# Performance work log

Hardware: AMD Instinct MI355X
Metric: run time of the kernel (lower is better)

Reference implementation:

```python
import math
import jax, jax.numpy as jnp
import numpy as np

B, T, E, H = 4, 2048, 256, 8
OBS_DIM, ACT_DIM = 17, 6
JOINED = OBS_DIM + ACT_DIM + 2  # 25: transition width in TAP trajectory transformer


def setup_inputs() -> dict:
    key = jax.random.key(0)
    ks = jax.random.split(key, 5)
    s = 0.02
    return {
        "x": jax.random.normal(ks[0], (B, T, E), dtype=jnp.float32),
        "Wq": jax.random.normal(ks[1], (E, E), dtype=jnp.float32) * s,
        "bq": jnp.zeros((E,), jnp.float32),
        "Wk": jax.random.normal(ks[2], (E, E), dtype=jnp.float32) * s,
        "bk": jnp.zeros((E,), jnp.float32),
        "Wv": jax.random.normal(ks[3], (E, E), dtype=jnp.float32) * s,
        "bv": jnp.zeros((E,), jnp.float32),
        "Wo": jax.random.normal(ks[4], (E, E), dtype=jnp.float32) * s,
        "bo": jnp.zeros((E,), jnp.float32),
    }


def _mask(t):
    # causal tril with every JOINED-th column (the "done"/boundary token) zeroed
    m = jnp.tril(jnp.ones((t, t), dtype=bool))
    keep_col = (jnp.arange(t) % JOINED) != (JOINED - 1)
    return m & keep_col[None, :]  # (t, t)


def reference(x, Wq, bq, Wk, bk, Wv, bv, Wo, bo):
    b, t, e = x.shape
    d = e // H
    # torch nn.Linear: y = x @ W.T + b
    q = (x @ Wq.T + bq).reshape(b, t, H, d).transpose(0, 2, 1, 3)  # b h t d
    k = (x @ Wk.T + bk).reshape(b, t, H, d).transpose(0, 2, 1, 3)
    v = (x @ Wv.T + bv).reshape(b, t, H, d).transpose(0, 2, 1, 3)

    scores = jnp.einsum("bhtd,bhsd->bhts", q, k) * (1.0 / math.sqrt(d))
    scores = jnp.where(_mask(t)[None, None], scores, -jnp.inf)
    attn = jax.nn.softmax(scores, axis=-1)  # (b, h, t, t) — dropout rate 0 => identity
    out = jnp.einsum("bhts,bhsd->bhtd", attn, v)  # b h t d
    out = out.transpose(0, 2, 1, 3).reshape(b, t, e)  # b t (h d)
    return out @ Wo.T + bo
```

## Files before the change

### kernel.cpp

```cpp
#include <hip/hip_runtime.h>

#define BB 4
#define TT 2048
#define EE 256
#define HH 8
#define DD 32
#define JOINED 25
#define CSCALE 0.2550539239731586f

typedef __attribute__((ext_vector_type(8))) __bf16 bf16x8;
typedef __attribute__((ext_vector_type(4))) float f32x4;

static __device__ __forceinline__ unsigned short f2bf(float f) {
    unsigned u = __float_as_uint(f);
    u += 0x7fffu + ((u >> 16) & 1u);
    return (unsigned short)(u >> 16);
}
static __device__ __forceinline__ unsigned pk2bf(float a, float b) {
    return (unsigned)f2bf(a) | ((unsigned)f2bf(b) << 16);
}

union BF8U { uint4 u; bf16x8 b; };
static __device__ __forceinline__ bf16x8 ld_frag(const unsigned short* p) {
    BF8U t; t.u = *(const uint4*)p; return t.b;
}

#define MFMA(a, b, c) __builtin_amdgcn_mfma_f32_16x16x32_bf16((a), (b), (c), 0, 0, 0)

__global__ __launch_bounds__(256) void prep_kernel(
    const float* __restrict__ x,
    const float* __restrict__ Wq, const float* __restrict__ Wk,
    const float* __restrict__ Wv, const float* __restrict__ Wo,
    unsigned short* __restrict__ xb, unsigned short* __restrict__ wqb,
    unsigned short* __restrict__ wkb, unsigned short* __restrict__ wvb,
    unsigned short* __restrict__ wob, unsigned short* __restrict__ onesG)
{
    const size_t NX = (size_t)BB * TT * EE;
    const size_t NMAIN = NX + 4 * (size_t)EE * EE;
    size_t idx = ((size_t)blockIdx.x * 256 + threadIdx.x) * 8;
    if (idx >= NMAIN) {
        size_t base = idx - NMAIN;
        #pragma unroll
        for (int i = 0; i < 8; ++i) {
            size_t e = base + i;
            if (e < (size_t)JOINED * 64) {
                int phase = (int)(e >> 6), o = (int)(e & 63);
                onesG[e] = (((phase + o) % JOINED) != (JOINED - 1)) ? (unsigned short)0x3F80
                                                                    : (unsigned short)0;
            }
        }
        return;
    }
    const float* src; unsigned short* dst; size_t off;
    if (idx < NX) { src = x; dst = xb; off = idx; }
    else {
        size_t i2 = idx - NX;
        int wsel = (int)(i2 >> 16);
        off = i2 & 65535u;
        src = wsel == 0 ? Wq : wsel == 1 ? Wk : wsel == 2 ? Wv : Wo;
        dst = wsel == 0 ? wqb : wsel == 1 ? wkb : wsel == 2 ? wvb : wob;
    }
    float4 a = *(const float4*)(src + off);
    float4 b = *(const float4*)(src + off + 4);
    uint4 o;
    o.x = pk2bf(a.x, a.y); o.y = pk2bf(a.z, a.w);
    o.z = pk2bf(b.x, b.y); o.w = pk2bf(b.z, b.w);
    *(uint4*)(dst + off) = o;
}

__global__ __launch_bounds__(256) void qkv_kernel(
    const unsigned short* __restrict__ xb,
    const unsigned short* __restrict__ wall,
    const float* __restrict__ bq, const float* __restrict__ bk,
    const float* __restrict__ bv,
    unsigned short* __restrict__ qo, unsigned short* __restrict__ ko,
    unsigned short* __restrict__ vto)
{
    __shared__ unsigned short As[128*136];
    __shared__ unsigned short Bs[128*136];

    const int m0 = blockIdx.x * 128;
    const int n0 = blockIdx.y * 128;
    const int which = blockIdx.y >> 1;
    const float* __restrict__ bias = which == 0 ? bq : which == 1 ? bk : bv;

    const int tid = threadIdx.x;
    const int w = tid >> 6, lane = tid & 63, quad = lane >> 4, lq = lane & 15;
    const int wm = (w & 1) * 64, wn = (w >> 1) * 64;
    const int srow = tid >> 4, scol = (tid & 15) * 8;

    f32x4 acc[4][4] = {};

    for (int k0 = 0; k0 < EE; k0 += 128) {
        __syncthreads();
        #pragma unroll
        for (int i = 0; i < 8; ++i) {
            int r = i * 16 + srow;
            *(uint4*)&As[r*136 + scol] = *(const uint4*)&xb  [(size_t)(m0 + r)*EE + k0 + scol];
            *(uint4*)&Bs[r*136 + scol] = *(const uint4*)&wall[(size_t)(n0 + r)*EE + k0 + scol];
        }
        __syncthreads();
        #pragma unroll
        for (int ks = 0; ks < 4; ++ks) {
            bf16x8 af[4], bfr[4];
            #pragma unroll
            for (int t = 0; t < 4; ++t) {
                af[t]  = ld_frag(&As[(wm + t*16 + lq)*136 + ks*32 + quad*8]);
                bfr[t] = ld_frag(&Bs[(wn + t*16 + lq)*136 + ks*32 + quad*8]);
            }
            #pragma unroll
            for (int mi = 0; mi < 4; ++mi)
                #pragma unroll
                for (int f = 0; f < 4; ++f)
                    acc[mi][f] = MFMA(af[mi], bfr[f], acc[mi][f]);
        }
    }

    #pragma unroll
    for (int f = 0; f < 4; ++f) {
        int nf = (n0 + wn + f*16 + lq) & 255;
        int h = nf >> 5, d = nf & 31;
        float bb = bias[nf];
        #pragma unroll
        for (int mi = 0; mi < 4; ++mi) {
            int t0 = m0 + wm + mi*16 + quad*4;
            int b = t0 >> 11, tl = t0 & (TT - 1);
            if (which == 0) {
                #pragma unroll
                for (int reg = 0; reg < 4; ++reg)
                    qo[(((size_t)b*HH + h)*TT + tl + reg)*DD + d] =
                        f2bf((acc[mi][f][reg] + bb) * CSCALE);
            } else if (which == 1) {
                #pragma unroll
                for (int reg = 0; reg < 4; ++reg)
                    ko[(((size_t)b*HH + h)*TT + tl + reg)*DD + d] =
                        f2bf(acc[mi][f][reg] + bb);
            } else {
                int r25 = tl % JOINED;
                int mreg = (JOINED - 1) - r25;
                float vv[4];
                #pragma unroll
                for (int reg = 0; reg < 4; ++reg)
                    vv[reg] = (reg == mreg) ? 0.f : (acc[mi][f][reg] + bb);
                uint2 pk;
                pk.x = pk2bf(vv[0], vv[1]);
                pk.y = pk2bf(vv[2], vv[3]);
                *(uint2*)&vto[(((size_t)b*HH + h)*DD + d)*TT + tl] = pk;
            }
        }
    }
}

__global__ __launch_bounds__(256, 4) void attn_kernel(
    const unsigned short* __restrict__ q, const unsigned short* __restrict__ k,
    const unsigned short* __restrict__ vt, const unsigned short* __restrict__ onesG,
    unsigned short* __restrict__ ao)
{
    __shared__ unsigned short Ks[2][64*40];
    __shared__ unsigned short Vt[2][32*72];
    __shared__ unsigned short Ps[4][16*72];

    const int L = blockIdx.x;
    const int xcd   = L & 7;
    const int inner = L >> 3;
    const int bh = xcd * 4 + (inner & 3);
    const int iq = 31 - (inner >> 2);
    const int b = bh >> 3, hh = bh & 7;

    const int tid = threadIdx.x;
    const int w = tid >> 6, lane = tid & 63, quad = lane >> 4, lq = lane & 15;
    const int r0 = iq * 64;
    const int q0 = r0 + w*16;
    const int ntiles = iq + 1;

    const int rk = tid >> 2, ck = (tid & 3) * 8;
    const int rv = tid >> 3, cv = (tid & 7) * 8;

    const unsigned short* qb_ = q  + (size_t)bh * TT * DD;
    const unsigned short* kb_ = k  + (size_t)bh * TT * DD;
    const unsigned short* vb_ = vt + (size_t)bh * DD * TT;

    const bf16x8 qf = ld_frag(qb_ + (size_t)(q0 + lq)*DD + quad*8);

    {
        uint4 kreg = *(const uint4*)(kb_ + (size_t)rk*DD + ck);
        uint4 vreg = *(const uint4*)(vb_ + (size_t)rv*TT + cv);
        *(uint4*)&Ks[0][rk*40 + ck] = kreg;
        *(uint4*)&Vt[0][rv*72 + cv] = vreg;
    }
    __syncthreads();

    f32x4 O0 = {0,0,0,0}, O1 = {0,0,0,0}, Ld = {0,0,0,0};
    int phase = 0;

    for (int jt = 0; jt < ntiles; ++jt) {
        const int j0 = jt * 64;
        const int jn = (jt + 1 < ntiles) ? j0 + 64 : j0;
        uint4 kreg = *(const uint4*)(kb_ + (size_t)(jn + rk)*DD + ck);
        uint4 vreg = *(const uint4*)(vb_ + (size_t)rv*TT + jn + cv);

        bf16x8 ones0 = ld_frag(&onesG[phase*64 +      quad*8]);
        bf16x8 ones1 = ld_frag(&onesG[phase*64 + 32 + quad*8]);

        const unsigned short* Kb = &Ks[jt & 1][0];
        const unsigned short* Vb = &Vt[jt & 1][0];

        f32x4 St[4];
        #pragma unroll
        for (int f = 0; f < 4; ++f) {
            bf16x8 kf = ld_frag(&Kb[(f*16 + lq)*40 + quad*8]);
            f32x4 z = {0,0,0,0};
            St[f] = MFMA(kf, qf, z);
        }
        if (jt == ntiles - 1) {
            int row = q0 + lq;
            #pragma unroll
            for (int f = 0; f < 4; ++f) {
                int kvb = j0 + f*16 + quad*4;
                #pragma unroll
                for (int reg = 0; reg < 4; ++reg)
                    St[f][reg] = (kvb + reg <= row) ? St[f][reg] : -1e30f;
            }
        }
        unsigned short* ps = &Ps[w][0];
        #pragma unroll
        for (int f = 0; f < 4; ++f) {
            float p0 = __builtin_amdgcn_exp2f(St[f][0]);
            float p1 = __builtin_amdgcn_exp2f(St[f][1]);
            float p2 = __builtin_amdgcn_exp2f(St[f][2]);
            float p3 = __builtin_amdgcn_exp2f(St[f][3]);
            uint2 pk;
            pk.x = pk2bf(p0, p1);
            pk.y = pk2bf(p2, p3);
            *(uint2*)&ps[lq*72 + f*16 + quad*4] = pk;
        }
        #pragma unroll
        for (int c = 0; c < 2; ++c) {
            bf16x8 pa  = ld_frag(&ps[lq*72 + c*32 + quad*8]);
            bf16x8 v0f = ld_frag(&Vb[(lq)*72      + c*32 + quad*8]);
            bf16x8 v1f = ld_frag(&Vb[(16 + lq)*72 + c*32 + quad*8]);
            O0 = MFMA(pa, v0f, O0);
            O1 = MFMA(pa, v1f, O1);
            Ld = MFMA(pa, (c ? ones1 : ones0), Ld);
        }

        *(uint4*)&Ks[(jt + 1) & 1][rk*40 + ck] = kreg;
        *(uint4*)&Vt[(jt + 1) & 1][rv*72 + cv] = vreg;
        __syncthreads();

        phase += 14; if (phase >= JOINED) phase -= JOINED;
    }

    #pragma unroll
    for (int reg = 0; reg < 4; ++reg) {
        float inv = 1.0f / Ld[reg];
        int t = q0 + quad*4 + reg;
        size_t ob = ((size_t)b*TT + t)*EE + hh*DD;
        ao[ob + lq]      = f2bf(O0[reg] * inv);
        ao[ob + 16 + lq] = f2bf(O1[reg] * inv);
    }
}

__global__ __launch_bounds__(256) void proj_kernel(
    const unsigned short* __restrict__ a, const unsigned short* __restrict__ W,
    const float* __restrict__ bias, float* __restrict__ out)
{
    __shared__ unsigned short As[128*136];
    __shared__ unsigned short Bs[128*136];

    const int m0 = blockIdx.x * 128;
    const int n0 = blockIdx.y * 128;
    const int tid = threadIdx.x;
    const int w = tid >> 6, lane = tid & 63, quad = lane >> 4, lq = lane & 15;
    const int wm = (w & 1) * 64, wn = (w >> 1) * 64;
    const int srow = tid >> 4, scol = (tid & 15) * 8;

    f32x4 acc[4][4] = {};

    for (int k0 = 0; k0 < EE; k0 += 128) {
        __syncthreads();
        #pragma unroll
        for (int i = 0; i < 8; ++i) {
            int r = i * 16 + srow;
            *(uint4*)&As[r*136 + scol] = *(const uint4*)&a[(size_t)(m0 + r)*EE + k0 + scol];
            *(uint4*)&Bs[r*136 + scol] = *(const uint4*)&W[(size_t)(n0 + r)*EE + k0 + scol];
        }
        __syncthreads();
        #pragma unroll
        for (int ks = 0; ks < 4; ++ks) {
            bf16x8 af[4], bfr[4];
            #pragma unroll
            for (int t = 0; t < 4; ++t) {
                af[t]  = ld_frag(&As[(wm + t*16 + lq)*136 + ks*32 + quad*8]);
                bfr[t] = ld_frag(&Bs[(wn + t*16 + lq)*136 + ks*32 + quad*8]);
            }
            #pragma unroll
            for (int mi = 0; mi < 4; ++mi)
                #pragma unroll
                for (int f = 0; f < 4; ++f)
                    acc[mi][f] = MFMA(af[mi], bfr[f], acc[mi][f]);
        }
    }

    #pragma unroll
    for (int f = 0; f < 4; ++f) {
        int n = n0 + wn + f*16 + lq;
        float bb = bias[n];
        #pragma unroll
        for (int mi = 0; mi < 4; ++mi) {
            int m = m0 + wm + mi*16 + quad*4;
            #pragma unroll
            for (int reg = 0; reg < 4; ++reg)
                out[(size_t)(m + reg)*EE + n] = acc[mi][f][reg] + bb;
        }
    }
}

extern "C" void kernel_launch(void* const* d_in, const int* in_sizes, int n_in,
                              void* d_out, int out_size, void* d_ws, size_t ws_size,
                              hipStream_t stream) {
    const float* x  = (const float*)d_in[0];
    const float* Wq = (const float*)d_in[1];
    const float* bq = (const float*)d_in[2];
    const float* Wk = (const float*)d_in[3];
    const float* bk = (const float*)d_in[4];
    const float* Wv = (const float*)d_in[5];
    const float* bv = (const float*)d_in[6];
    const float* Wo = (const float*)d_in[7];
    const float* bo = (const float*)d_in[8];
    float* out = (float*)d_out;

    const size_t n_elem = (size_t)BB * TT * EE;
    const size_t w_elem = (size_t)EE * EE;
    unsigned short* xb    = (unsigned short*)d_ws;
    unsigned short* wqb   = xb  + n_elem;
    unsigned short* wkb   = wqb + w_elem;
    unsigned short* wvb   = wkb + w_elem;
    unsigned short* wob   = wvb + w_elem;
    unsigned short* qq    = wob + w_elem;
    unsigned short* kk    = qq  + n_elem;
    unsigned short* vtt   = kk  + n_elem;
    unsigned short* ao    = vtt + n_elem;
    unsigned short* onesG = ao  + n_elem;

    const int prep_blocks = (int)((n_elem + 4*w_elem) / 2048) + 1;
    prep_kernel<<<dim3(prep_blocks), 256, 0, stream>>>(
        x, Wq, Wk, Wv, Wo, xb, wqb, wkb, wvb, wob, onesG);
    qkv_kernel <<<dim3(BB*TT/128, 6), 256, 0, stream>>>(
        xb, wqb, bq, bk, bv, qq, kk, vtt);
    attn_kernel<<<dim3(1024), 256, 0, stream>>>(qq, kk, vtt, onesG, ao);
    proj_kernel<<<dim3(BB*TT/128, EE/128), 256, 0, stream>>>(ao, wob, bo, out);
}
```

Measured before the change: 120.5 us.

## Split causal attention KV range into chunks with a separate merge kernel

The attention kernel now splits each query tile's key range into chunks of up to 8 KV tiles, giving 2560 blocks of roughly equal work instead of 1024 blocks with very uneven causal lengths. Each block writes unnormalized fp32 partial outputs and row sums to a workspace buffer. A new merge kernel adds the partials and normalizes before the output projection. Because softmax is computed without a running max, the partials can simply be summed. The costs are extra global traffic for the partials, one more kernel launch, and dropping the previous XCD-aware block ordering.

```diff
diff --git a/kernel.cpp b/kernel.cpp
--- a/kernel.cpp
+++ b/kernel.cpp
@@ -7,6 +7,9 @@
 #define DD 32
 #define JOINED 25
 #define CSCALE 0.2550539239731586f
+#define PROW 33
+#define PCHUNK (64*PROW)
+#define PART_OFF (64u << 20)
 
 typedef __attribute__((ext_vector_type(8))) __bf16 bf16x8;
 typedef __attribute__((ext_vector_type(4))) float f32x4;
@@ -154,24 +157,27 @@
 __global__ __launch_bounds__(256, 4) void attn_kernel(
     const unsigned short* __restrict__ q, const unsigned short* __restrict__ k,
     const unsigned short* __restrict__ vt, const unsigned short* __restrict__ onesG,
-    unsigned short* __restrict__ ao)
+    float* __restrict__ part)
 {
     __shared__ unsigned short Ks[2][64*40];
     __shared__ unsigned short Vt[2][32*72];
     __shared__ unsigned short Ps[4][16*72];
 
     const int L = blockIdx.x;
-    const int xcd   = L & 7;
-    const int inner = L >> 3;
-    const int bh = xcd * 4 + (inner & 3);
-    const int iq = 31 - (inner >> 2);
-    const int b = bh >> 3, hh = bh & 7;
+    const int bh = L & 31;
+    const int widx = L >> 5;
+    int iq, c;
+    if (widx < 8)       { iq = widx;               c = 0; }
+    else if (widx < 24) { int t = widx - 8;  iq = 8  + (t >> 1); c = t & 1; }
+    else if (widx < 48) { int t = widx - 24; iq = 16 + t / 3;    c = t % 3; }
+    else                { int t = widx - 48; iq = 24 + (t >> 2); c = t & 3; }
+    const int tstart = c * 8;
+    const int tend = min(tstart + 8, iq + 1);
 
     const int tid = threadIdx.x;
     const int w = tid >> 6, lane = tid & 63, quad = lane >> 4, lq = lane & 15;
     const int r0 = iq * 64;
     const int q0 = r0 + w*16;
-    const int ntiles = iq + 1;
 
     const int rk = tid >> 2, ck = (tid & 3) * 8;
     const int rv = tid >> 3, cv = (tid & 7) * 8;
@@ -183,19 +189,19 @@
     const bf16x8 qf = ld_frag(qb_ + (size_t)(q0 + lq)*DD + quad*8);
 
     {
-        uint4 kreg = *(const uint4*)(kb_ + (size_t)rk*DD + ck);
-        uint4 vreg = *(const uint4*)(vb_ + (size_t)rv*TT + cv);
+        uint4 kreg = *(const uint4*)(kb_ + (size_t)(tstart*64 + rk)*DD + ck);
+        uint4 vreg = *(const uint4*)(vb_ + (size_t)rv*TT + tstart*64 + cv);
         *(uint4*)&Ks[0][rk*40 + ck] = kreg;
         *(uint4*)&Vt[0][rv*72 + cv] = vreg;
     }
     __syncthreads();
 
     f32x4 O0 = {0,0,0,0}, O1 = {0,0,0,0}, Ld = {0,0,0,0};
-    int phase = 0;
-
-    for (int jt = 0; jt < ntiles; ++jt) {
+    int phase = (tstart * 64) % JOINED;
+
+    for (int jt = tstart; jt < tend; ++jt) {
         const int j0 = jt * 64;
-        const int jn = (jt + 1 < ntiles) ? j0 + 64 : j0;
+        const int jn = (jt + 1 < tend) ? j0 + 64 : j0;
         uint4 kreg = *(const uint4*)(kb_ + (size_t)(jn + rk)*DD + ck);
         uint4 vreg = *(const uint4*)(vb_ + (size_t)rv*TT + jn + cv);
 
@@ -212,7 +218,7 @@
             f32x4 z = {0,0,0,0};
             St[f] = MFMA(kf, qf, z);
         }
-        if (jt == ntiles - 1) {
+        if (jt == iq) {
             int row = q0 + lq;
             #pragma unroll
             for (int f = 0; f < 4; ++f) {
@@ -235,13 +241,13 @@
             *(uint2*)&ps[lq*72 + f*16 + quad*4] = pk;
         }
         #pragma unroll
-        for (int c = 0; c < 2; ++c) {
-            bf16x8 pa  = ld_frag(&ps[lq*72 + c*32 + quad*8]);
-            bf16x8 v0f = ld_frag(&Vb[(lq)*72      + c*32 + quad*8]);
-            bf16x8 v1f = ld_frag(&Vb[(16 + lq)*72 + c*32 + quad*8]);
+        for (int cc = 0; cc < 2; ++cc) {
+            bf16x8 pa  = ld_frag(&ps[lq*72 + cc*32 + quad*8]);
+            bf16x8 v0f = ld_frag(&Vb[(lq)*72      + cc*32 + quad*8]);
+            bf16x8 v1f = ld_frag(&Vb[(16 + lq)*72 + cc*32 + quad*8]);
             O0 = MFMA(pa, v0f, O0);
             O1 = MFMA(pa, v1f, O1);
-            Ld = MFMA(pa, (c ? ones1 : ones0), Ld);
+            Ld = MFMA(pa, (cc ? ones1 : ones0), Ld);
         }
 
         *(uint4*)&Ks[(jt + 1) & 1][rk*40 + ck] = kreg;
@@ -251,14 +257,37 @@
         phase += 14; if (phase >= JOINED) phase -= JOINED;
     }
 
+    float* pb = part + ((size_t)(bh*32 + iq)*4 + c) * PCHUNK;
     #pragma unroll
     for (int reg = 0; reg < 4; ++reg) {
-        float inv = 1.0f / Ld[reg];
-        int t = q0 + quad*4 + reg;
-        size_t ob = ((size_t)b*TT + t)*EE + hh*DD;
-        ao[ob + lq]      = f2bf(O0[reg] * inv);
-        ao[ob + 16 + lq] = f2bf(O1[reg] * inv);
-    }
+        int row = w*16 + quad*4 + reg;
+        pb[row*PROW + lq]      = O0[reg];
+        pb[row*PROW + 16 + lq] = O1[reg];
+        if (lq == 0) pb[row*PROW + 32] = Ld[reg];
+    }
+}
+
+__global__ __launch_bounds__(256) void merge_kernel(
+    const float* __restrict__ part, unsigned short* __restrict__ ao)
+{
+    int gid = blockIdx.x * 256 + threadIdx.x;
+    int rowg = gid >> 4;
+    int dp = gid & 15;
+    int bh = rowg >> 11, t = rowg & 2047;
+    int iq = t >> 6, rl = t & 63;
+    int nc = (iq >> 3) + 1;
+    const float* pb = part + ((size_t)(bh*32 + iq)*4) * PCHUNK + rl*PROW;
+    float s0 = 0.f, s1 = 0.f, sl = 0.f;
+    for (int c = 0; c < nc; ++c) {
+        const float* p = pb + c*PCHUNK;
+        s0 += p[dp*2];
+        s1 += p[dp*2 + 1];
+        sl += p[32];
+    }
+    float inv = 1.0f / sl;
+    int b = bh >> 3, h = bh & 7;
+    unsigned pk = pk2bf(s0 * inv, s1 * inv);
+    *(unsigned*)&ao[((size_t)b*TT + t)*EE + h*DD + dp*2] = pk;
 }
 
 __global__ __launch_bounds__(256) void proj_kernel(
@@ -342,12 +371,14 @@
     unsigned short* vtt   = kk  + n_elem;
     unsigned short* ao    = vtt + n_elem;
     unsigned short* onesG = ao  + n_elem;
+    float* part = (float*)((char*)d_ws + PART_OFF);
 
     const int prep_blocks = (int)((n_elem + 4*w_elem) / 2048) + 1;
     prep_kernel<<<dim3(prep_blocks), 256, 0, stream>>>(
         x, Wq, Wk, Wv, Wo, xb, wqb, wkb, wvb, wob, onesG);
     qkv_kernel <<<dim3(BB*TT/128, 6), 256, 0, stream>>>(
         xb, wqb, bq, bk, bv, qq, kk, vtt);
-    attn_kernel<<<dim3(1024), 256, 0, stream>>>(qq, kk, vtt, onesG, ao);
+    attn_kernel<<<dim3(2560), 256, 0, stream>>>(qq, kk, vtt, onesG, part);
+    merge_kernel<<<dim3(4096), 256, 0, stream>>>(part, ao);
     proj_kernel<<<dim3(BB*TT/128, EE/128), 256, 0, stream>>>(ao, wob, bo, out);
 }
```

After: 122.5 us. Within noise of the previous version (+1.7%).
